# Optimization experiments

Hardware: AMD Instinct MI355X
Metric: run time of the kernel (lower is better)

The kernel has to match this reference:

```python
import jax, jax.numpy as jnp
import numpy as np

B, T, C = 4, 2048, 1024
H, D = 16, 64  # n_heads, head_dim; C == H*D

def setup_inputs() -> dict:
    key = jax.random.key(0)
    ks = jax.random.split(key, 6)
    s_in = 1.0 / np.sqrt(C)
    x = jax.random.normal(ks[0], (B, T, C), dtype=jnp.float32)
    # causal mask: True above the diagonal -> masked to -inf
    mask = jnp.triu(jnp.ones((T, T), dtype=bool), k=1)
    Wqkv = jax.random.uniform(ks[1], (C, 3 * C), jnp.float32, -s_in, s_in)
    bqkv = jax.random.uniform(ks[2], (3 * C,), jnp.float32, -s_in, s_in)
    Wout = jax.random.uniform(ks[3], (C, C), jnp.float32, -s_in, s_in)
    bout = jax.random.uniform(ks[4], (C,), jnp.float32, -s_in, s_in)
    return {"x": x, "mask": mask, "Wqkv": Wqkv, "bqkv": bqkv, "Wout": Wout, "bout": bout}

def reference(x, mask, Wqkv, bqkv, Wout, bout):
    b, t, c = x.shape
    qkv = (x @ Wqkv + bqkv).reshape(b, t, 3, H, D)
    qkv = jnp.transpose(qkv, (2, 0, 3, 1, 4))  # [3, B, H, T, D]
    q, k, v = qkv[0], qkv[1], qkv[2]
    scores = jnp.einsum("bhqd,bhkd->bhqk", q, k) / jnp.sqrt(jnp.float32(D))
    scores = jnp.where(mask[:t, :t][None, None, :, :], -jnp.inf, scores)
    attn = jax.nn.softmax(scores, axis=-1)
    out = jnp.einsum("bhqk,bhkd->bhqd", attn, v)
    out = jnp.transpose(out, (0, 2, 1, 3)).reshape(b, t, c)
    return out @ Wout + bout
```

## Files before the change

### kernel.cpp

```cpp
#include <hip/hip_runtime.h>

typedef unsigned short u16;
typedef __attribute__((ext_vector_type(8))) short bf16x8;
typedef __attribute__((ext_vector_type(4))) short bf16x4;
typedef __attribute__((ext_vector_type(4))) float f32x4;

#define MFMA16(a, b, c) __builtin_amdgcn_mfma_f32_16x16x32_bf16(a, b, c, 0, 0, 0)

__device__ __forceinline__ u16 f2bf(float x) {
    unsigned u = __float_as_uint(x);
    return (u16)((u + 0x7fffu + ((u >> 16) & 1u)) >> 16);
}
__device__ __forceinline__ u16 f2bf_fast(float x) {
    return (u16)((__float_as_uint(x) + 0x8000u) >> 16);
}

__global__ __launch_bounds__(256) void castk(const float* __restrict__ src, u16* __restrict__ dst) {
    const int i = (blockIdx.x * 256 + threadIdx.x) * 8;
    float4 a = *(const float4*)(src + i);
    float4 b = *(const float4*)(src + i + 4);
    bf16x8 v;
    v[0] = (short)f2bf(a.x); v[1] = (short)f2bf(a.y);
    v[2] = (short)f2bf(a.z); v[3] = (short)f2bf(a.w);
    v[4] = (short)f2bf(b.x); v[5] = (short)f2bf(b.y);
    v[6] = (short)f2bf(b.z); v[7] = (short)f2bf(b.w);
    *(bf16x8*)(dst + i) = v;
}

__global__ __launch_bounds__(256) void tkern(const float* __restrict__ src, u16* __restrict__ dst,
                                             int R, int C) {
    const int tC = C >> 6;
    const int tr = (blockIdx.x / tC) << 6;
    const int tc = (blockIdx.x % tC) << 6;
    __shared__ u16 ls[64 * 68];
    const int tid = threadIdx.x;
#pragma unroll
    for (int rep = 0; rep < 2; ++rep) {
        const int f = tid * 8 + rep * 2048;
        const int r = f >> 6, c = f & 63;
        float4 a = *(const float4*)(src + (size_t)(tr + r) * C + tc + c);
        float4 b = *(const float4*)(src + (size_t)(tr + r) * C + tc + c + 4);
        bf16x4 lo, hi;
        lo[0] = (short)f2bf(a.x); lo[1] = (short)f2bf(a.y);
        lo[2] = (short)f2bf(a.z); lo[3] = (short)f2bf(a.w);
        hi[0] = (short)f2bf(b.x); hi[1] = (short)f2bf(b.y);
        hi[2] = (short)f2bf(b.z); hi[3] = (short)f2bf(b.w);
        *(bf16x4*)&ls[r * 68 + c] = lo;
        *(bf16x4*)&ls[r * 68 + c + 4] = hi;
    }
    __syncthreads();
#pragma unroll
    for (int rep = 0; rep < 2; ++rep) {
        const int f = tid * 8 + rep * 2048;
        const int rn = f >> 6, ck = f & 63;
        bf16x8 v;
#pragma unroll
        for (int j = 0; j < 8; ++j) v[j] = (short)ls[(ck + j) * 68 + rn];
        *(bf16x8*)(dst + (size_t)(tc + rn) * R + tr + ck) = v;
    }
}

template <int MODE>
__global__ __launch_bounds__(256) void gemm_k(const u16* __restrict__ A, const u16* __restrict__ Bt,
                                              const float* __restrict__ bias,
                                              u16* __restrict__ Qo, u16* __restrict__ Ko,
                                              u16* __restrict__ Vo, float* __restrict__ Of) {
    constexpr int Kd = 1024;
    const int tid = threadIdx.x;
    const int lane = tid & 63, wave = tid >> 6;
    const int wm = wave >> 1, wn = wave & 1;
    const int lr = lane & 15, lg = lane >> 4;
    const int mt = blockIdx.x & 63;
    const int nt = blockIdx.x >> 6;
    const int mbase = mt << 7, nbase = nt << 7;
    __shared__ u16 As[128 * 32];
    __shared__ u16 Bs[128 * 32];
    f32x4 acc[4][4];
#pragma unroll
    for (int i = 0; i < 4; ++i)
#pragma unroll
        for (int j = 0; j < 4; ++j) acc[i][j] = {0.f, 0.f, 0.f, 0.f};

    for (int kb = 0; kb < Kd; kb += 32) {
        __syncthreads();
#pragma unroll
        for (int rep = 0; rep < 2; ++rep) {
            const int f = tid * 8 + rep * 2048;
            const int r = f >> 5, c = f & 31;
            __builtin_amdgcn_global_load_lds(
                (const __attribute__((address_space(1))) void*)(A + (size_t)(mbase + r) * Kd + kb + c),
                (__attribute__((address_space(3))) void*)(As + f), 16, 0, 0);
            __builtin_amdgcn_global_load_lds(
                (const __attribute__((address_space(1))) void*)(Bt + (size_t)(nbase + r) * Kd + kb + c),
                (__attribute__((address_space(3))) void*)(Bs + f), 16, 0, 0);
        }
        __syncthreads();
        bf16x8 af[4], bfr[4];
#pragma unroll
        for (int i = 0; i < 4; ++i)
            af[i] = *(const bf16x8*)&As[(wm * 64 + i * 16 + lr) * 32 + lg * 8];
#pragma unroll
        for (int j = 0; j < 4; ++j)
            bfr[j] = *(const bf16x8*)&Bs[(wn * 64 + j * 16 + lr) * 32 + lg * 8];
#pragma unroll
        for (int i = 0; i < 4; ++i)
#pragma unroll
            for (int j = 0; j < 4; ++j) acc[i][j] = MFMA16(af[i], bfr[j], acc[i][j]);
    }

    const float QSCALE = 0.1803368801111137f;
#pragma unroll
    for (int j = 0; j < 4; ++j) {
        const int n = nbase + wn * 64 + j * 16 + lr;
        const float bj = bias[n];
        if (MODE == 0) {
            const int three = n >> 10;
            const int h = (n >> 6) & 15;
            const int d = n & 63;
#pragma unroll
            for (int i = 0; i < 4; ++i) {
#pragma unroll
                for (int r = 0; r < 4; ++r) {
                    const int m = mbase + wm * 64 + i * 16 + lg * 4 + r;
                    const int b = m >> 11, t = m & 2047;
                    const int bh = (b << 4) + h;
                    const float val = acc[i][j][r] + bj;
                    if (three == 0)
                        Qo[(((size_t)bh << 11) + t) * 64 + d] = f2bf(val * QSCALE);
                    else if (three == 1)
                        Ko[(((size_t)bh << 11) + t) * 64 + d] = f2bf(val);
                    else
                        Vo[(((size_t)bh << 6) + d) * 2048 + t] = f2bf(val);
                }
            }
        } else {
#pragma unroll
            for (int i = 0; i < 4; ++i) {
#pragma unroll
                for (int r = 0; r < 4; ++r) {
                    const int m = mbase + wm * 64 + i * 16 + lg * 4 + r;
                    Of[((size_t)m << 10) + n] = acc[i][j][r] + bj;
                }
            }
        }
    }
}

__global__ __launch_bounds__(128, 2) void flash_attn(const u16* __restrict__ Q, const u16* __restrict__ Kg,
                                                     const u16* __restrict__ Vt, u16* __restrict__ Aout) {
    const int tid = threadIdx.x;
    const int lane = tid & 63, wave = tid >> 6;
    const int lr = lane & 15, lg = lane >> 4;
    const int bx = blockIdx.x;
    const int bh = blockIdx.y;
    const int b = bh >> 4, h = bh & 15;
    const size_t base = (size_t)bh << 17;

    const int qb_hi = 16 + bx;
    const int qb_lo = 15 - bx;

    __shared__ u16 Ps[2][16 * 72];

    int qbase[4];
    qbase[0] = qb_hi * 64 + wave * 32;
    qbase[1] = qbase[0] + 16;
    qbase[2] = qb_lo * 64 + wave * 32;
    qbase[3] = qbase[2] + 16;

    bf16x8 qf[4][2];
#pragma unroll
    for (int st = 0; st < 4; ++st) {
        const u16* p = Q + base + (size_t)(qbase[st] + lr) * 64;
        qf[st][0] = *(const bf16x8*)(p + lg * 8);
        qf[st][1] = *(const bf16x8*)(p + 32 + lg * 8);
    }

    f32x4 o[4][4];
#pragma unroll
    for (int st = 0; st < 4; ++st)
#pragma unroll
        for (int dt = 0; dt < 4; ++dt) o[st][dt] = {0.f, 0.f, 0.f, 0.f};
    float m_[4] = {-INFINITY, -INFINITY, -INFINITY, -INFINITY};
    float l_[4] = {0.f, 0.f, 0.f, 0.f};

    const u16* Kbase = Kg + base + (size_t)lr * 64 + lg * 8;
    const u16* Vbase = Vt + base + (size_t)lr * 2048 + lg * 8;

    for (int kt = 0; kt <= qb_hi; ++kt) {
        bf16x8 kf[4][2], vf[4][2];
        const u16* kp = Kbase + (size_t)kt * 4096;
#pragma unroll
        for (int rt = 0; rt < 4; ++rt) {
            kf[rt][0] = *(const bf16x8*)(kp + rt * 1024);
            kf[rt][1] = *(const bf16x8*)(kp + rt * 1024 + 32);
        }
        const u16* vp = Vbase + kt * 64;
#pragma unroll
        for (int dt = 0; dt < 4; ++dt) {
            vf[dt][0] = *(const bf16x8*)(vp + dt * 32768);
            vf[dt][1] = *(const bf16x8*)(vp + dt * 32768 + 32);
        }

        auto process = [&](int st, bool diag) {
            f32x4 s[4];
#pragma unroll
            for (int rt = 0; rt < 4; ++rt) {
                f32x4 z = {0.f, 0.f, 0.f, 0.f};
                z = MFMA16(kf[rt][0], qf[st][0], z);
                z = MFMA16(kf[rt][1], qf[st][1], z);
                s[rt] = z;
            }
            if (diag) {
                const int q_glob = qbase[st] + lr;
#pragma unroll
                for (int rt = 0; rt < 4; ++rt)
#pragma unroll
                    for (int r = 0; r < 4; ++r) {
                        const int kv = kt * 64 + rt * 16 + lg * 4 + r;
                        if (kv > q_glob) s[rt][r] = -INFINITY;
                    }
            }
            float rmax = -INFINITY;
#pragma unroll
            for (int rt = 0; rt < 4; ++rt)
#pragma unroll
                for (int r = 0; r < 4; ++r) rmax = fmaxf(rmax, s[rt][r]);
            rmax = fmaxf(rmax, __shfl_xor(rmax, 16));
            rmax = fmaxf(rmax, __shfl_xor(rmax, 32));
            const float m_new = fmaxf(m_[st], rmax);
            const float alpha = exp2f(m_[st] - m_new);
            float rsum = 0.f;
#pragma unroll
            for (int rt = 0; rt < 4; ++rt)
#pragma unroll
                for (int r = 0; r < 4; ++r) {
                    const float p = exp2f(s[rt][r] - m_new);
                    s[rt][r] = p;
                    rsum += p;
                }
            rsum += __shfl_xor(rsum, 16);
            rsum += __shfl_xor(rsum, 32);
            l_[st] = l_[st] * alpha + rsum;
            m_[st] = m_new;

#pragma unroll
            for (int rt = 0; rt < 4; ++rt) {
                bf16x4 pk;
#pragma unroll
                for (int r = 0; r < 4; ++r) pk[r] = (short)f2bf_fast(s[rt][r]);
                *(bf16x4*)&Ps[wave][lr * 72 + rt * 16 + lg * 4] = pk;
            }
            float aq[4];
#pragma unroll
            for (int r = 0; r < 4; ++r) aq[r] = __shfl(alpha, (lane & 48) + lg * 4 + r);
#pragma unroll
            for (int dt = 0; dt < 4; ++dt)
#pragma unroll
                for (int r = 0; r < 4; ++r) o[st][dt][r] *= aq[r];

            const bf16x8 pf0 = *(const bf16x8*)&Ps[wave][lr * 72 + lg * 8];
            const bf16x8 pf1 = *(const bf16x8*)&Ps[wave][lr * 72 + 32 + lg * 8];
#pragma unroll
            for (int dt = 0; dt < 4; ++dt) {
                o[st][dt] = MFMA16(pf0, vf[dt][0], o[st][dt]);
                o[st][dt] = MFMA16(pf1, vf[dt][1], o[st][dt]);
            }
        };

        process(0, kt == qb_hi);
        process(1, kt == qb_hi);
        if (kt <= qb_lo) {
            process(2, kt == qb_lo);
            process(3, kt == qb_lo);
        }
    }

#pragma unroll
    for (int st = 0; st < 4; ++st) {
        const float linv = 1.f / l_[st];
        float lq[4];
#pragma unroll
        for (int r = 0; r < 4; ++r) lq[r] = __shfl(linv, (lane & 48) + lg * 4 + r);
#pragma unroll
        for (int dt = 0; dt < 4; ++dt)
#pragma unroll
            for (int r = 0; r < 4; ++r) {
                const int t = qbase[st] + lg * 4 + r;
                Aout[(((size_t)(b << 11) + t) << 10) + h * 64 + dt * 16 + lr] =
                    f2bf(o[st][dt][r] * lq[r]);
            }
    }
}

extern "C" void kernel_launch(void* const* d_in, const int* in_sizes, int n_in,
                              void* d_out, int out_size, void* d_ws, size_t ws_size,
                              hipStream_t stream) {
    (void)in_sizes; (void)n_in; (void)out_size; (void)ws_size;
    const float* x    = (const float*)d_in[0];
    const float* Wqkv = (const float*)d_in[2];
    const float* bqkv = (const float*)d_in[3];
    const float* Wout = (const float*)d_in[4];
    const float* bout = (const float*)d_in[5];
    float* out = (float*)d_out;

    char* ws = (char*)d_ws;
    u16* WqkvT = (u16*)(ws);
    u16* WoutT = (u16*)(ws + 6291456);
    u16* xb    = (u16*)(ws + 8388608);
    u16* Qb    = (u16*)(ws + 25165824);
    u16* Kb    = (u16*)(ws + 41943040);
    u16* Vtb   = (u16*)(ws + 58720256);
    u16* Ab    = (u16*)(ws + 75497472);

    castk<<<dim3(4096), 256, 0, stream>>>(x, xb);
    tkern<<<dim3(16 * 48), 256, 0, stream>>>(Wqkv, WqkvT, 1024, 3072);
    tkern<<<dim3(16 * 16), 256, 0, stream>>>(Wout, WoutT, 1024, 1024);
    gemm_k<0><<<dim3(64 * 24), 256, 0, stream>>>(xb, WqkvT, bqkv, Qb, Kb, Vtb, nullptr);
    flash_attn<<<dim3(16, 64), 128, 0, stream>>>(Qb, Kb, Vtb, Ab);
    gemm_k<1><<<dim3(64 * 8), 256, 0, stream>>>(Ab, WoutT, bout, nullptr, nullptr, nullptr, out);
}
```

Before: 345.1 us.

## Double-buffer K/V register tiles and alternate P shared buffers per subtile

Measured after the change: 590.1 us. +71.0%, slower.

```diff
diff --git a/kernel.cpp b/kernel.cpp
--- a/kernel.cpp
+++ b/kernel.cpp
@@ -159,7 +159,7 @@
     const int qb_hi = 16 + bx;
     const int qb_lo = 15 - bx;
 
-    __shared__ u16 Ps[2][16 * 72];
+    __shared__ u16 Ps[2][2][16 * 72];
 
     int qbase[4];
     qbase[0] = qb_hi * 64 + wave * 32;
@@ -186,8 +186,7 @@
     const u16* Kbase = Kg + base + (size_t)lr * 64 + lg * 8;
     const u16* Vbase = Vt + base + (size_t)lr * 2048 + lg * 8;
 
-    for (int kt = 0; kt <= qb_hi; ++kt) {
-        bf16x8 kf[4][2], vf[4][2];
+    auto loadkv = [&](bf16x8 (&kf)[4][2], bf16x8 (&vf)[4][2], int kt) {
         const u16* kp = Kbase + (size_t)kt * 4096;
 #pragma unroll
         for (int rt = 0; rt < 4; ++rt) {
@@ -200,79 +199,95 @@
             vf[dt][0] = *(const bf16x8*)(vp + dt * 32768);
             vf[dt][1] = *(const bf16x8*)(vp + dt * 32768 + 32);
         }
-
-        auto process = [&](int st, bool diag) {
-            f32x4 s[4];
-#pragma unroll
-            for (int rt = 0; rt < 4; ++rt) {
-                f32x4 z = {0.f, 0.f, 0.f, 0.f};
-                z = MFMA16(kf[rt][0], qf[st][0], z);
-                z = MFMA16(kf[rt][1], qf[st][1], z);
-                s[rt] = z;
+    };
+
+    auto process = [&](const bf16x8 (&kf)[4][2], const bf16x8 (&vf)[4][2], int kt, int st,
+                       bool diag) {
+        f32x4 s[4];
+#pragma unroll
+        for (int rt = 0; rt < 4; ++rt) {
+            f32x4 z = {0.f, 0.f, 0.f, 0.f};
+            z = MFMA16(kf[rt][0], qf[st][0], z);
+            z = MFMA16(kf[rt][1], qf[st][1], z);
+            s[rt] = z;
+        }
+        if (diag) {
+            const int q_glob = qbase[st] + lr;
+#pragma unroll
+            for (int rt = 0; rt < 4; ++rt)
+#pragma unroll
+                for (int r = 0; r < 4; ++r) {
+                    const int kv = kt * 64 + rt * 16 + lg * 4 + r;
+                    if (kv > q_glob) s[rt][r] = -INFINITY;
+                }
+        }
+        float rmax = -INFINITY;
+#pragma unroll
+        for (int rt = 0; rt < 4; ++rt)
+#pragma unroll
+            for (int r = 0; r < 4; ++r) rmax = fmaxf(rmax, s[rt][r]);
+        rmax = fmaxf(rmax, __shfl_xor(rmax, 16));
+        rmax = fmaxf(rmax, __shfl_xor(rmax, 32));
+        const float m_new = fmaxf(m_[st], rmax);
+        const float alpha = exp2f(m_[st] - m_new);
+        float rsum = 0.f;
+#pragma unroll
+        for (int rt = 0; rt < 4; ++rt)
+#pragma unroll
+            for (int r = 0; r < 4; ++r) {
+                const float p = exp2f(s[rt][r] - m_new);
+                s[rt][r] = p;
+                rsum += p;
             }
-            if (diag) {
-                const int q_glob = qbase[st] + lr;
-#pragma unroll
-                for (int rt = 0; rt < 4; ++rt)
-#pragma unroll
-                    for (int r = 0; r < 4; ++r) {
-                        const int kv = kt * 64 + rt * 16 + lg * 4 + r;
-                        if (kv > q_glob) s[rt][r] = -INFINITY;
-                    }
-            }
-            float rmax = -INFINITY;
-#pragma unroll
-            for (int rt = 0; rt < 4; ++rt)
-#pragma unroll
-                for (int r = 0; r < 4; ++r) rmax = fmaxf(rmax, s[rt][r]);
-            rmax = fmaxf(rmax, __shfl_xor(rmax, 16));
-            rmax = fmaxf(rmax, __shfl_xor(rmax, 32));
-            const float m_new = fmaxf(m_[st], rmax);
-            const float alpha = exp2f(m_[st] - m_new);
-            float rsum = 0.f;
-#pragma unroll
-            for (int rt = 0; rt < 4; ++rt)
-#pragma unroll
-                for (int r = 0; r < 4; ++r) {
-                    const float p = exp2f(s[rt][r] - m_new);
-                    s[rt][r] = p;
-                    rsum += p;
-                }
-            rsum += __shfl_xor(rsum, 16);
-            rsum += __shfl_xor(rsum, 32);
-            l_[st] = l_[st] * alpha + rsum;
-            m_[st] = m_new;
-
-#pragma unroll
-            for (int rt = 0; rt < 4; ++rt) {
-                bf16x4 pk;
-#pragma unroll
-                for (int r = 0; r < 4; ++r) pk[r] = (short)f2bf_fast(s[rt][r]);
-                *(bf16x4*)&Ps[wave][lr * 72 + rt * 16 + lg * 4] = pk;
-            }
-            float aq[4];
-#pragma unroll
-            for (int r = 0; r < 4; ++r) aq[r] = __shfl(alpha, (lane & 48) + lg * 4 + r);
-#pragma unroll
-            for (int dt = 0; dt < 4; ++dt)
-#pragma unroll
-                for (int r = 0; r < 4; ++r) o[st][dt][r] *= aq[r];
-
-            const bf16x8 pf0 = *(const bf16x8*)&Ps[wave][lr * 72 + lg * 8];
-            const bf16x8 pf1 = *(const bf16x8*)&Ps[wave][lr * 72 + 32 + lg * 8];
-#pragma unroll
-            for (int dt = 0; dt < 4; ++dt) {
-                o[st][dt] = MFMA16(pf0, vf[dt][0], o[st][dt]);
-                o[st][dt] = MFMA16(pf1, vf[dt][1], o[st][dt]);
-            }
-        };
-
-        process(0, kt == qb_hi);
-        process(1, kt == qb_hi);
+        rsum += __shfl_xor(rsum, 16);
+        rsum += __shfl_xor(rsum, 32);
+        l_[st] = l_[st] * alpha + rsum;
+        m_[st] = m_new;
+
+        u16* psb = &Ps[wave][st & 1][0];
+#pragma unroll
+        for (int rt = 0; rt < 4; ++rt) {
+            bf16x4 pk;
+#pragma unroll
+            for (int r = 0; r < 4; ++r) pk[r] = (short)f2bf_fast(s[rt][r]);
+            *(bf16x4*)&psb[lr * 72 + rt * 16 + lg * 4] = pk;
+        }
+        float aq[4];
+#pragma unroll
+        for (int r = 0; r < 4; ++r) aq[r] = __shfl(alpha, (lane & 48) + lg * 4 + r);
+#pragma unroll
+        for (int dt = 0; dt < 4; ++dt)
+#pragma unroll
+            for (int r = 0; r < 4; ++r) o[st][dt][r] *= aq[r];
+
+        const bf16x8 pf0 = *(const bf16x8*)&psb[lr * 72 + lg * 8];
+        const bf16x8 pf1 = *(const bf16x8*)&psb[lr * 72 + 32 + lg * 8];
+#pragma unroll
+        for (int dt = 0; dt < 4; ++dt) {
+            o[st][dt] = MFMA16(pf0, vf[dt][0], o[st][dt]);
+            o[st][dt] = MFMA16(pf1, vf[dt][1], o[st][dt]);
+        }
+    };
+
+    auto step = [&](const bf16x8 (&kf)[4][2], const bf16x8 (&vf)[4][2], int kt) {
+        process(kf, vf, kt, 0, kt == qb_hi);
+        process(kf, vf, kt, 1, kt == qb_hi);
         if (kt <= qb_lo) {
-            process(2, kt == qb_lo);
-            process(3, kt == qb_lo);
-        }
+            process(kf, vf, kt, 2, kt == qb_lo);
+            process(kf, vf, kt, 3, kt == qb_lo);
+        }
+    };
+
+    bf16x8 kfA[4][2], vfA[4][2], kfB[4][2], vfB[4][2];
+    loadkv(kfA, vfA, 0);
+    int kt = 0;
+    for (;;) {
+        if (kt < qb_hi) loadkv(kfB, vfB, kt + 1);
+        step(kfA, vfA, kt);
+        if (++kt > qb_hi) break;
+        if (kt < qb_hi) loadkv(kfA, vfA, kt + 1);
+        step(kfB, vfB, kt);
+        if (++kt > qb_hi) break;
     }
 
 #pragma unroll
```
